# Performance work log

Hardware: AMD Instinct MI355X
Metric: run time of the kernel (lower is better)

## Reference

```python
import jax, jax.numpy as jnp
import numpy as np

# Dimensions (see shape_source): input_size L=8192, n_variates C=10, bag_ratio=0.14
B, L, C = 512, 8192, 10
BAG = int(0.14 * L)        # 1146  (kernel_size of grouped conv)
STRIDE = BAG // 4          # 286
N_OUT = 10                 # conv out_channels (== groups, 1 filter per variate)
POOL = 3                   # MaxPool1d kernel (stride defaults to kernel)
N_CLASSES = 10             # output_size
L_OUT = (L - BAG) // STRIDE + 1   # 25
L_P = L_OUT // POOL               # 8  -> 8 * N_OUT == 80 fc input features


def setup_inputs() -> dict:
    key = jax.random.key(0)
    k1, k2, k3 = jax.random.split(key, 3)
    x = jax.random.normal(k1, (B, L, C), dtype=jnp.float32)
    conv_bias = jax.random.normal(k2, (N_OUT,), dtype=jnp.float32) * 0.02
    fc_w = jax.random.normal(k3, (N_CLASSES, N_OUT * L_P), dtype=jnp.float32) * 0.05
    fc_b = jnp.zeros((N_CLASSES,), dtype=jnp.float32)
    return {"x": x, "conv_bias": conv_bias, "fc_w": fc_w, "fc_b": fc_b}


def reference(x, conv_bias, fc_w, fc_b):
    # torch does x.view(B, shape[2], shape[1]) -> a RESHAPE, not a transpose.
    xb = jnp.reshape(x, (B, C, L))
    # Grouped Conv1d with frozen all-ones weights == strided sliding-window sum.
    # Exploit this with an exclusive cumsum (O(N) instead of O(N*K)).
    cs = jnp.concatenate([jnp.zeros((B, C, 1), xb.dtype), jnp.cumsum(xb, axis=-1)], axis=-1)  # [B,C,L+1]
    starts = jnp.arange(L_OUT) * STRIDE
    win_sum = cs[:, :, starts + BAG] - cs[:, :, starts]          # [B, C, L_OUT]
    y = (win_sum + conv_bias[None, :, None]) ** 2                # conv + bias, squared
    neg = -y
    # MaxPool1d(kernel=3, stride=3): floor division trims the tail element.
    pooled = neg[:, :, : L_P * POOL].reshape(B, N_OUT, L_P, POOL).max(axis=-1)  # [B,10,8]
    flat = pooled.reshape(B, N_OUT * L_P)                        # [B, 80]
    return flat @ fc_w.T + fc_b
```

## Files before the change

### kernel.cpp

```cpp
#include <hip/hip_runtime.h>

#define BATCH   512
#define LEN     8192
#define NCH     10
#define BAG     1146
#define STRIDE  286
#define L_OUT   25
#define POOLK   3
#define L_P     8
#define NCLS    10
#define NFEAT   (NCH * L_P)

__global__ __launch_bounds__(256) void conv_win_kernel(
    const float* __restrict__ x, const float* __restrict__ conv_bias,
    float* __restrict__ neg_out) {
    const int bc = blockIdx.x;
    const int c  = bc % NCH;

    __shared__ float s[LEN];

    const float4* row4 = (const float4*)(x + (size_t)bc * LEN);
    float4* s4 = (float4*)s;
#pragma unroll
    for (int i = 0; i < (LEN / 4) / 256; ++i) {
        s4[threadIdx.x + i * 256] = row4[threadIdx.x + i * 256];
    }
    __syncthreads();

    const int wave = threadIdx.x >> 6;
    const int lane = threadIdx.x & 63;
    const float bias = conv_bias[c];

    for (int o = wave; o < L_OUT; o += 4) {
        const int start = o * STRIDE;
        float sum = 0.f;
        for (int k = lane; k < BAG; k += 64) sum += s[start + k];
#pragma unroll
        for (int off = 32; off > 0; off >>= 1) sum += __shfl_xor(sum, off);
        if (lane == 0) {
            const float v = sum + bias;
            neg_out[bc * L_OUT + o] = -(v * v);
        }
    }
}

__global__ __launch_bounds__(128) void pool_fc_kernel(
    const float* __restrict__ neg, const float* __restrict__ fc_w,
    const float* __restrict__ fc_b, float* __restrict__ out) {
    const int b = blockIdx.x;
    const int t = threadIdx.x;
    __shared__ float flat[NFEAT];

    if (t < NFEAT) {
        const int c = t >> 3;
        const int p = t & 7;
        const float* n = neg + (size_t)(b * NCH + c) * L_OUT + p * POOLK;
        flat[t] = fmaxf(fmaxf(n[0], n[1]), n[2]);
    }
    __syncthreads();

    if (t < NCLS) {
        float acc = fc_b[t];
#pragma unroll
        for (int f = 0; f < NFEAT; ++f) acc += flat[f] * fc_w[t * NFEAT + f];
        out[b * NCLS + t] = acc;
    }
}

extern "C" void kernel_launch(void* const* d_in, const int* in_sizes, int n_in,
                              void* d_out, int out_size, void* d_ws, size_t ws_size,
                              hipStream_t stream) {
    const float* x         = (const float*)d_in[0];
    const float* conv_bias = (const float*)d_in[1];
    const float* fc_w      = (const float*)d_in[2];
    const float* fc_b      = (const float*)d_in[3];
    float* out = (float*)d_out;
    float* neg = (float*)d_ws;

    conv_win_kernel<<<BATCH * NCH, 256, 0, stream>>>(x, conv_bias, neg);
    pool_fc_kernel<<<BATCH, 128, 0, stream>>>(neg, fc_w, fc_b, out);
}
```

Baseline: 237.3 us.

## Decompose sliding windows into shared stride segments summed once

The window length is four strides plus two elements. The kernel therefore sums each of the 28 stride-length segments once per row, with one wave per segment, and records each segment's first two elements. Each output is then built from four segment sums plus those two elements. This removes the roughly fourfold redundant summation and the 32 KB LDS staging per block. Loads now go straight from global memory as float2, and the unused row tail is never read. In exchange, the float summation order changes.

```diff
diff --git a/kernel.cpp b/kernel.cpp
--- a/kernel.cpp
+++ b/kernel.cpp
@@ -11,36 +11,47 @@
 #define NCLS    10
 #define NFEAT   (NCH * L_P)
 
-__global__ __launch_bounds__(256) void conv_win_kernel(
+__global__ __launch_bounds__(256) void seg_win_kernel(
     const float* __restrict__ x, const float* __restrict__ conv_bias,
     float* __restrict__ neg_out) {
     const int bc = blockIdx.x;
     const int c  = bc % NCH;
+    const float* row = x + (size_t)bc * LEN;
 
-    __shared__ float s[LEN];
+    __shared__ float S[28];
+    __shared__ float F2[29];
 
-    const float4* row4 = (const float4*)(x + (size_t)bc * LEN);
-    float4* s4 = (float4*)s;
+    const int wave = threadIdx.x >> 6;
+    const int lane = threadIdx.x & 63;
+
+    for (int j = wave; j < 29; j += 4) {
+        const float2* p2 = (const float2*)(row + j * STRIDE);
+        float2 v0 = make_float2(0.f, 0.f);
+        float2 v1 = make_float2(0.f, 0.f);
+        float2 v2 = make_float2(0.f, 0.f);
+        if (j < 28) {
+            v0 = p2[lane];
+            v1 = p2[lane + 64];
+            if (lane < 15) v2 = p2[lane + 128];
+        } else if (lane == 0) {
+            v0 = p2[0];
+        }
+        const float f2v = v0.x + v0.y;
+        float sum = (v0.x + v0.y) + (v1.x + v1.y) + (v2.x + v2.y);
 #pragma unroll
-    for (int i = 0; i < (LEN / 4) / 256; ++i) {
-        s4[threadIdx.x + i * 256] = row4[threadIdx.x + i * 256];
+        for (int off = 32; off > 0; off >>= 1) sum += __shfl_xor(sum, off);
+        if (lane == 0) {
+            if (j < 28) S[j] = sum;
+            F2[j] = f2v;
+        }
     }
     __syncthreads();
 
-    const int wave = threadIdx.x >> 6;
-    const int lane = threadIdx.x & 63;
-    const float bias = conv_bias[c];
-
-    for (int o = wave; o < L_OUT; o += 4) {
-        const int start = o * STRIDE;
-        float sum = 0.f;
-        for (int k = lane; k < BAG; k += 64) sum += s[start + k];
-#pragma unroll
-        for (int off = 32; off > 0; off >>= 1) sum += __shfl_xor(sum, off);
-        if (lane == 0) {
-            const float v = sum + bias;
-            neg_out[bc * L_OUT + o] = -(v * v);
-        }
+    const int t = threadIdx.x;
+    if (t < L_OUT) {
+        const float w = S[t] + S[t + 1] + S[t + 2] + S[t + 3] + F2[t + 4]
+                        + conv_bias[c];
+        neg_out[bc * L_OUT + t] = -(w * w);
     }
 }
 
@@ -77,6 +88,6 @@
     float* out = (float*)d_out;
     float* neg = (float*)d_ws;
 
-    conv_win_kernel<<<BATCH * NCH, 256, 0, stream>>>(x, conv_bias, neg);
+    seg_win_kernel<<<BATCH * NCH, 256, 0, stream>>>(x, conv_bias, neg);
     pool_fc_kernel<<<BATCH, 128, 0, stream>>>(neg, fc_w, fc_b, out);
 }
```

Result: no change. 234.5 us (-1.2%).
